# Kernel optimization log

Measured on AMD Instinct MI355X. Metric: run time of the kernel, lower is better.

The kernel has to match this reference:

```python
import jax, jax.numpy as jnp
import numpy as np
from jax import lax
from jax.scipy.special import logsumexp

B, N = 8, 2048
EPS = 0.2      # entropic regularization for Sinkhorn-EMD
ITERS = 20     # Sinkhorn iterations (CUDA EMD kernel is likewise an approximate matcher)


def setup_inputs() -> dict:
    key = jax.random.key(0)
    k1, k2 = jax.random.split(key)
    target = jax.random.normal(k1, (B, N, 3), dtype=jnp.float32)
    pre = jax.random.normal(k2, (B, N, 3), dtype=jnp.float32)
    return {"target": target, "pre": pre}


def _pairwise_sq(x, y):
    # x: [B,N,3], y: [B,M,3] -> squared L2 distances [B,N,M]
    xx = jnp.sum(x * x, axis=-1)                      # [B,N]
    yy = jnp.sum(y * y, axis=-1)                      # [B,M]
    xy = jnp.einsum('bnd,bmd->bnm', x, y)             # [B,N,M]
    return xx[:, :, None] + yy[:, None, :] - 2.0 * xy


def _total_loss(target, pre):
    C = _pairwise_sq(pre, target)                     # [B,N,M] cost: squared dists
    n, m = C.shape[1], C.shape[2]

    # Chamfer: chamfer_3DDist returns squared NN distances both ways.
    dist1 = jnp.min(C, axis=2)                        # pre -> target, [B,N]
    dist2 = jnp.min(C, axis=1)                        # target -> pre, [B,M]
    # per-sample cd = mean(dist1) + 0.5*mean(dist2), summed over batch
    cd_total = jnp.sum(jnp.mean(dist1, axis=1) + 0.5 * jnp.mean(dist2, axis=1))

    # EMD via entropic OT (Sinkhorn, log-domain) with uniform marginals.
    log_a = -jnp.log(jnp.float32(n))
    log_b = -jnp.log(jnp.float32(m))
    f0 = jnp.zeros((C.shape[0], n), dtype=C.dtype)
    g0 = jnp.zeros((C.shape[0], m), dtype=C.dtype)

    def step(carry, _):
        f, g = carry
        f = -EPS * logsumexp((g[:, None, :] - C) / EPS + log_b, axis=2)
        g = -EPS * logsumexp((f[:, :, None] - C) / EPS + log_a, axis=1)
        return (f, g), None

    (f, g), _ = lax.scan(step, (f0, g0), None, length=ITERS)
    logP = (f[:, :, None] + g[:, None, :] - C) / EPS + log_a + log_b
    # CUDA earth_mover_distance returns sum of matched squared dists per sample;
    # OT plan rows carry mass 1/n, so scale by n to get the per-point matching sum.
    emd_b = jnp.float32(n) * jnp.sum(jnp.exp(logP) * C, axis=(1, 2))  # [B]
    emd_loss = jnp.sum(emd_b)

    return cd_total + emd_loss


def reference(target, pre):
    return _total_loss(target, pre)
```

## Files before the change

### kernel.cpp

```cpp
#include <hip/hip_runtime.h>
#include <math.h>

#define NTHREADS 512
#define NPTS 2048
#define MSTEPS (NPTS / 64)
#define RPW 4
#define NWAVES (NTHREADS / 64)
#define ROWS_PER_BLOCK (NWAVES * RPW)
#define BLKB (NPTS / ROWS_PER_BLOCK)
#define BATCH 8
#define NBLOCKS (BATCH * BLKB)
#define SINK_ITERS 20

#if __has_builtin(__builtin_amdgcn_exp2f)
#define EXP2(x) __builtin_amdgcn_exp2f(x)
#else
#define EXP2(x) exp2f(x)
#endif

#define S2F 7.21347520444482f
#define LB2 -11.0f
#define FINAL_SCALE (0.13862943611198906f / 2048.0f)

#define WS_PART  0
#define WS_DONE  2048
#define WS_F     4096
#define WS_G     (WS_F    + 4 * BATCH * NPTS)
#define WS_CMIN  (WS_G    + 4 * BATCH * NPTS)
#define WS_PT    (WS_CMIN + 4 * BATCH * NPTS)
#define WS_PP    (WS_PT   + 16 * BATCH * NPTS)

static __device__ __forceinline__ float aload(const float* p) {
  return __hip_atomic_load(p, __ATOMIC_RELAXED, __HIP_MEMORY_SCOPE_AGENT);
}
static __device__ __forceinline__ unsigned aloadu(const unsigned* p) {
  return __hip_atomic_load(p, __ATOMIC_RELAXED, __HIP_MEMORY_SCOPE_AGENT);
}

__global__ void __launch_bounds__(256, 4)
prep_kernel(const float* __restrict__ target, const float* __restrict__ pre,
            unsigned char* __restrict__ ws)
{
  float4*   PT   = (float4*)(ws + WS_PT);
  float4*   PP   = (float4*)(ws + WS_PP);
  float*    F    = (float*)(ws + WS_F);
  float*    G    = (float*)(ws + WS_G);
  unsigned* CMIN = (unsigned*)(ws + WS_CMIN);
  unsigned* done = (unsigned*)(ws + WS_DONE);

  const float S1 = sqrtf(S2F);
  int gid = blockIdx.x * 256 + threadIdx.x;
  if (gid == 0) *done = 0u;
  if (gid < BATCH * NPTS) {
    const float* p = target + (size_t)gid * 3;
    float y0 = p[0] * S1, y1 = p[1] * S1, y2 = p[2] * S1;
    PT[gid] = make_float4(y0, y1, y2, y0 * y0 + y1 * y1 + y2 * y2);
    const float* q = pre + (size_t)gid * 3;
    float z0 = q[0] * S1, z1 = q[1] * S1, z2 = q[2] * S1;
    PP[gid] = make_float4(z0, z1, z2, z0 * z0 + z1 * z1 + z2 * z2);
    F[gid] = 0.0f;
    G[gid] = 0.0f;
    CMIN[gid] = 0x7f800000u;
  }
}

template<int MODE>
__global__ void __launch_bounds__(NTHREADS, 4)
sink_kernel(const float4* __restrict__ rowpts, const float4* __restrict__ colpts,
            const float* __restrict__ Vin, float* __restrict__ Vout,
            unsigned char* __restrict__ ws, float* __restrict__ out)
{
  float*    partial = (float*)(ws + WS_PART);
  unsigned* done    = (unsigned*)(ws + WS_DONE);
  unsigned* CMIN    = (unsigned*)(ws + WS_CMIN);

  __shared__ float4 cols4[NPTS];
  __shared__ float  W2[NPTS];
  __shared__ float  wsum[NWAVES];
  __shared__ int    isLast;

  const int tid  = threadIdx.x;
  const int wid  = tid >> 6;
  const int lane = tid & 63;
  const int b    = blockIdx.x / BLKB;
  const int bib  = blockIdx.x % BLKB;

  const float4* rb = rowpts + (size_t)b * NPTS;
  const float4* cb = colpts + (size_t)b * NPTS;
  const float*  Vi = (MODE == 1) ? nullptr : (Vin + (size_t)b * NPTS);
  float*        Vo = (MODE == 2) ? nullptr : (Vout + (size_t)b * NPTS);
  unsigned*     CMb = CMIN + (size_t)b * NPTS;

  for (int m = tid; m < NPTS; m += NTHREADS) {
    float4 p = cb[m];
    float w;
    if (MODE == 1) {
      w = LB2 - p.w;
      ((unsigned*)W2)[m] = 0x7f800000u;
    } else {
      float v = Vi[m];
      w = v - p.w + LB2;
      if (MODE == 2) W2[m] = v + LB2;
    }
    cols4[m] = make_float4(p.x, p.y, p.z, w);
  }
  __syncthreads();

  const int n0 = bib * ROWS_PER_BLOCK + wid * RPW;
  float x2[RPW][3], XX[RPW], S[RPW], tm[RPW], Sc[RPW];
#pragma unroll
  for (int r = 0; r < RPW; ++r) {
    float4 a = rb[n0 + r];
    XX[r] = a.w;
    x2[r][0] = a.x + a.x; x2[r][1] = a.y + a.y; x2[r][2] = a.z + a.z;
    S[r] = 0.0f;
    if (MODE == 1) tm[r] = -3.0e38f;
    if (MODE == 2) Sc[r] = 0.0f;
  }

#pragma unroll 2
  for (int ms = 0; ms < MSTEPS; ++ms) {
    float4 v = cols4[ms * 64 + lane];
    float w2;
    if (MODE == 2) w2 = W2[ms * 64 + lane];
    float tmax;
    if (MODE == 1) tmax = -3.0e38f;
#pragma unroll
    for (int r = 0; r < RPW; ++r) {
      float t = v.w - XX[r];
      t = fmaf(x2[r][0], v.x, t);
      t = fmaf(x2[r][1], v.y, t);
      t = fmaf(x2[r][2], v.z, t);
      float e = EXP2(t);
      S[r] += e;
      if (MODE == 1) { tm[r] = fmaxf(tm[r], t); tmax = fmaxf(tmax, t); }
      if (MODE == 2) { Sc[r] = fmaf(e, w2 - t, Sc[r]); }
    }
    if (MODE == 1)
      atomicMin((unsigned*)&W2[ms * 64 + lane], __float_as_uint(LB2 - tmax));
  }

  float rowacc = 0.0f;
#pragma unroll
  for (int r = 0; r < RPW; ++r) {
    float s = S[r];
    for (int off = 32; off; off >>= 1) s += __shfl_xor(s, off);
    if (MODE != 2) {
      if (lane == r) Vo[n0 + r] = -log2f(s);
    } else {
      float sc = Sc[r];
      for (int off = 32; off; off >>= 1) sc += __shfl_xor(sc, off);
      rowacc += 2048.0f * (sc / s);
    }
    if (MODE == 1) {
      float t = tm[r];
      for (int off = 32; off; off >>= 1) t = fmaxf(t, __shfl_xor(t, off));
      rowacc += LB2 - t;
    }
  }

  if (MODE == 1) {
    if (lane == 0) wsum[wid] = rowacc;
    __syncthreads();
    if (tid == 0) {
      float s = 0.0f;
#pragma unroll
      for (int w = 0; w < NWAVES; ++w) s += wsum[w];
      partial[blockIdx.x] = s;
    }
    for (int m = tid; m < NPTS; m += NTHREADS)
      atomicMin(&CMb[m], ((unsigned*)W2)[m]);
  }

  if (MODE == 2) {
    if (lane == 0) wsum[wid] = rowacc;
    __syncthreads();
    if (tid == 0) {
      float s = 0.0f;
#pragma unroll
      for (int w = 0; w < NWAVES; ++w) s += wsum[w];
      partial[blockIdx.x] += s;
      __threadfence();
      unsigned old = __hip_atomic_fetch_add(done, 1u, __ATOMIC_ACQ_REL,
                                            __HIP_MEMORY_SCOPE_AGENT);
      isLast = (old == (unsigned)NBLOCKS - 1u) ? 1 : 0;
    }
    __syncthreads();
    if (isLast) {
      float s = aload(&partial[tid]);
      for (int j = tid; j < BATCH * NPTS; j += NTHREADS)
        s += 0.5f * __uint_as_float(aloadu(&CMIN[j]));
      for (int off = 32; off; off >>= 1) s += __shfl_xor(s, off);
      if (lane == 0) wsum[wid] = s;
      __syncthreads();
      if (tid == 0) {
        float t = 0.0f;
#pragma unroll
        for (int w = 0; w < NWAVES; ++w) t += wsum[w];
        out[0] = t * FINAL_SCALE;
      }
    }
  }
}

extern "C" void kernel_launch(void* const* d_in, const int* in_sizes, int n_in,
                              void* d_out, int out_size, void* d_ws, size_t ws_size,
                              hipStream_t stream) {
  const float* target = (const float*)d_in[0];
  const float* pre    = (const float*)d_in[1];
  float* out = (float*)d_out;
  unsigned char* ws = (unsigned char*)d_ws;

  const float4* PT = (const float4*)(ws + WS_PT);
  const float4* PP = (const float4*)(ws + WS_PP);
  float* F = (float*)(ws + WS_F);
  float* G = (float*)(ws + WS_G);

  prep_kernel<<<dim3((BATCH * NPTS + 255) / 256), dim3(256), 0, stream>>>(target, pre, ws);

  sink_kernel<1><<<dim3(NBLOCKS), dim3(NTHREADS), 0, stream>>>(PP, PT, nullptr, F, ws, nullptr);
  sink_kernel<0><<<dim3(NBLOCKS), dim3(NTHREADS), 0, stream>>>(PT, PP, F, G, ws, nullptr);

  for (int it = 1; it < SINK_ITERS; ++it) {
    sink_kernel<0><<<dim3(NBLOCKS), dim3(NTHREADS), 0, stream>>>(PP, PT, G, F, ws, nullptr);
    if (it < SINK_ITERS - 1) {
      sink_kernel<0><<<dim3(NBLOCKS), dim3(NTHREADS), 0, stream>>>(PT, PP, F, G, ws, nullptr);
    } else {
      sink_kernel<2><<<dim3(NBLOCKS), dim3(NTHREADS), 0, stream>>>(PT, PP, F, nullptr, ws, out);
    }
  }
}
```

Baseline: 469.1 us.

## Fuse prep into first Sinkhorn pass and compute column Chamfer min in final pass

Removes the separate prep kernel: the first Sinkhorn kernel now reads the raw target/pre points, scales them, writes the packed float4 arrays for its own rows, and builds its column tile in shared memory. The target->pre Chamfer minimum is no longer gathered with per-column shared and global atomicMin plus a global CMIN buffer. It is computed as a per-row min in the final MODE 2 pass, which already iterates over the transposed orientation. This drops one launch, the CMIN init and readback, and the atomics, at the cost of extra fmin work in the last pass.

```diff
diff --git a/kernel.cpp b/kernel.cpp
--- a/kernel.cpp
+++ b/kernel.cpp
@@ -26,41 +26,94 @@
 #define WS_DONE  2048
 #define WS_F     4096
 #define WS_G     (WS_F    + 4 * BATCH * NPTS)
-#define WS_CMIN  (WS_G    + 4 * BATCH * NPTS)
-#define WS_PT    (WS_CMIN + 4 * BATCH * NPTS)
+#define WS_PT    (WS_G    + 4 * BATCH * NPTS)
 #define WS_PP    (WS_PT   + 16 * BATCH * NPTS)
 
 static __device__ __forceinline__ float aload(const float* p) {
   return __hip_atomic_load(p, __ATOMIC_RELAXED, __HIP_MEMORY_SCOPE_AGENT);
 }
-static __device__ __forceinline__ unsigned aloadu(const unsigned* p) {
-  return __hip_atomic_load(p, __ATOMIC_RELAXED, __HIP_MEMORY_SCOPE_AGENT);
-}
-
-__global__ void __launch_bounds__(256, 4)
-prep_kernel(const float* __restrict__ target, const float* __restrict__ pre,
-            unsigned char* __restrict__ ws)
+
+__global__ void __launch_bounds__(NTHREADS, 4)
+sink_first_kernel(const float* __restrict__ target, const float* __restrict__ pre,
+                  unsigned char* __restrict__ ws)
 {
-  float4*   PT   = (float4*)(ws + WS_PT);
-  float4*   PP   = (float4*)(ws + WS_PP);
-  float*    F    = (float*)(ws + WS_F);
-  float*    G    = (float*)(ws + WS_G);
-  unsigned* CMIN = (unsigned*)(ws + WS_CMIN);
-  unsigned* done = (unsigned*)(ws + WS_DONE);
-
+  float*    partial = (float*)(ws + WS_PART);
+  unsigned* done    = (unsigned*)(ws + WS_DONE);
+  float*    F       = (float*)(ws + WS_F);
+  float4*   PT      = (float4*)(ws + WS_PT);
+  float4*   PP      = (float4*)(ws + WS_PP);
+
+  __shared__ float4 cols4[NPTS];
+  __shared__ float  wsum[NWAVES];
+
+  const int tid  = threadIdx.x;
+  const int wid  = tid >> 6;
+  const int lane = tid & 63;
+  const int b    = blockIdx.x / BLKB;
+  const int bib  = blockIdx.x % BLKB;
   const float S1 = sqrtf(S2F);
-  int gid = blockIdx.x * 256 + threadIdx.x;
-  if (gid == 0) *done = 0u;
-  if (gid < BATCH * NPTS) {
-    const float* p = target + (size_t)gid * 3;
+
+  if (blockIdx.x == 0 && tid == 0) *done = 0u;
+
+  const float*  tb = target + (size_t)b * NPTS * 3;
+  const float*  pb = pre    + (size_t)b * NPTS * 3;
+  const unsigned mlo = (unsigned)(bib * ROWS_PER_BLOCK);
+
+  for (int m = tid; m < NPTS; m += NTHREADS) {
+    const float* p = tb + m * 3;
     float y0 = p[0] * S1, y1 = p[1] * S1, y2 = p[2] * S1;
-    PT[gid] = make_float4(y0, y1, y2, y0 * y0 + y1 * y1 + y2 * y2);
-    const float* q = pre + (size_t)gid * 3;
-    float z0 = q[0] * S1, z1 = q[1] * S1, z2 = q[2] * S1;
-    PP[gid] = make_float4(z0, z1, z2, z0 * z0 + z1 * z1 + z2 * z2);
-    F[gid] = 0.0f;
-    G[gid] = 0.0f;
-    CMIN[gid] = 0x7f800000u;
+    float yy = y0 * y0 + y1 * y1 + y2 * y2;
+    if ((unsigned)m - mlo < (unsigned)ROWS_PER_BLOCK)
+      PT[(size_t)b * NPTS + m] = make_float4(y0, y1, y2, yy);
+    cols4[m] = make_float4(y0, y1, y2, LB2 - yy);
+  }
+
+  const int n0 = (int)mlo + wid * RPW;
+  float x2[RPW][3], XX[RPW], S[RPW], tm[RPW];
+#pragma unroll
+  for (int r = 0; r < RPW; ++r) {
+    const float* q = pb + (size_t)(n0 + r) * 3;
+    float a0 = q[0] * S1, a1 = q[1] * S1, a2 = q[2] * S1;
+    float xx = a0 * a0 + a1 * a1 + a2 * a2;
+    if (lane == r) PP[(size_t)b * NPTS + n0 + r] = make_float4(a0, a1, a2, xx);
+    XX[r] = xx;
+    x2[r][0] = a0 + a0; x2[r][1] = a1 + a1; x2[r][2] = a2 + a2;
+    S[r] = 0.0f; tm[r] = -3.0e38f;
+  }
+  __syncthreads();
+
+#pragma unroll 2
+  for (int ms = 0; ms < MSTEPS; ++ms) {
+    float4 v = cols4[ms * 64 + lane];
+#pragma unroll
+    for (int r = 0; r < RPW; ++r) {
+      float t = v.w - XX[r];
+      t = fmaf(x2[r][0], v.x, t);
+      t = fmaf(x2[r][1], v.y, t);
+      t = fmaf(x2[r][2], v.z, t);
+      S[r] += EXP2(t);
+      tm[r] = fmaxf(tm[r], t);
+    }
+  }
+
+  float rowacc = 0.0f;
+  float* Fb = F + (size_t)b * NPTS;
+#pragma unroll
+  for (int r = 0; r < RPW; ++r) {
+    float s = S[r];
+    for (int off = 32; off; off >>= 1) s += __shfl_xor(s, off);
+    if (lane == r) Fb[n0 + r] = -log2f(s);
+    float t = tm[r];
+    for (int off = 32; off; off >>= 1) t = fmaxf(t, __shfl_xor(t, off));
+    rowacc += LB2 - t;
+  }
+  if (lane == 0) wsum[wid] = rowacc;
+  __syncthreads();
+  if (tid == 0) {
+    float s = 0.0f;
+#pragma unroll
+    for (int w = 0; w < NWAVES; ++w) s += wsum[w];
+    partial[blockIdx.x] = s;
   }
 }
 
@@ -72,10 +125,9 @@
 {
   float*    partial = (float*)(ws + WS_PART);
   unsigned* done    = (unsigned*)(ws + WS_DONE);
-  unsigned* CMIN    = (unsigned*)(ws + WS_CMIN);
 
   __shared__ float4 cols4[NPTS];
-  __shared__ float  W2[NPTS];
+  __shared__ float  W2[MODE == 2 ? NPTS : 1];
   __shared__ float  wsum[NWAVES];
   __shared__ int    isLast;
 
@@ -87,35 +139,26 @@
 
   const float4* rb = rowpts + (size_t)b * NPTS;
   const float4* cb = colpts + (size_t)b * NPTS;
-  const float*  Vi = (MODE == 1) ? nullptr : (Vin + (size_t)b * NPTS);
+  const float*  Vi = Vin + (size_t)b * NPTS;
   float*        Vo = (MODE == 2) ? nullptr : (Vout + (size_t)b * NPTS);
-  unsigned*     CMb = CMIN + (size_t)b * NPTS;
 
   for (int m = tid; m < NPTS; m += NTHREADS) {
     float4 p = cb[m];
-    float w;
-    if (MODE == 1) {
-      w = LB2 - p.w;
-      ((unsigned*)W2)[m] = 0x7f800000u;
-    } else {
-      float v = Vi[m];
-      w = v - p.w + LB2;
-      if (MODE == 2) W2[m] = v + LB2;
-    }
-    cols4[m] = make_float4(p.x, p.y, p.z, w);
+    float v = Vi[m];
+    if (MODE == 2) W2[m] = v + LB2;
+    cols4[m] = make_float4(p.x, p.y, p.z, v - p.w + LB2);
   }
   __syncthreads();
 
   const int n0 = bib * ROWS_PER_BLOCK + wid * RPW;
-  float x2[RPW][3], XX[RPW], S[RPW], tm[RPW], Sc[RPW];
+  float x2[RPW][3], XX[RPW], S[RPW], Sc[RPW], rm2[RPW];
 #pragma unroll
   for (int r = 0; r < RPW; ++r) {
     float4 a = rb[n0 + r];
     XX[r] = a.w;
     x2[r][0] = a.x + a.x; x2[r][1] = a.y + a.y; x2[r][2] = a.z + a.z;
     S[r] = 0.0f;
-    if (MODE == 1) tm[r] = -3.0e38f;
-    if (MODE == 2) Sc[r] = 0.0f;
+    if (MODE == 2) { Sc[r] = 0.0f; rm2[r] = 3.0e38f; }
   }
 
 #pragma unroll 2
@@ -123,8 +166,6 @@
     float4 v = cols4[ms * 64 + lane];
     float w2;
     if (MODE == 2) w2 = W2[ms * 64 + lane];
-    float tmax;
-    if (MODE == 1) tmax = -3.0e38f;
 #pragma unroll
     for (int r = 0; r < RPW; ++r) {
       float t = v.w - XX[r];
@@ -133,11 +174,12 @@
       t = fmaf(x2[r][2], v.z, t);
       float e = EXP2(t);
       S[r] += e;
-      if (MODE == 1) { tm[r] = fmaxf(tm[r], t); tmax = fmaxf(tmax, t); }
-      if (MODE == 2) { Sc[r] = fmaf(e, w2 - t, Sc[r]); }
-    }
-    if (MODE == 1)
-      atomicMin((unsigned*)&W2[ms * 64 + lane], __float_as_uint(LB2 - tmax));
+      if (MODE == 2) {
+        float c2 = w2 - t;
+        Sc[r] = fmaf(e, c2, Sc[r]);
+        rm2[r] = fminf(rm2[r], c2);
+      }
+    }
   }
 
   float rowacc = 0.0f;
@@ -150,26 +192,10 @@
     } else {
       float sc = Sc[r];
       for (int off = 32; off; off >>= 1) sc += __shfl_xor(sc, off);
-      rowacc += 2048.0f * (sc / s);
-    }
-    if (MODE == 1) {
-      float t = tm[r];
-      for (int off = 32; off; off >>= 1) t = fmaxf(t, __shfl_xor(t, off));
-      rowacc += LB2 - t;
-    }
-  }
-
-  if (MODE == 1) {
-    if (lane == 0) wsum[wid] = rowacc;
-    __syncthreads();
-    if (tid == 0) {
-      float s = 0.0f;
-#pragma unroll
-      for (int w = 0; w < NWAVES; ++w) s += wsum[w];
-      partial[blockIdx.x] = s;
-    }
-    for (int m = tid; m < NPTS; m += NTHREADS)
-      atomicMin(&CMb[m], ((unsigned*)W2)[m]);
+      float m2 = rm2[r];
+      for (int off = 32; off; off >>= 1) m2 = fminf(m2, __shfl_xor(m2, off));
+      rowacc += 2048.0f * (sc / s) + 0.5f * m2;
+    }
   }
 
   if (MODE == 2) {
@@ -188,8 +214,6 @@
     __syncthreads();
     if (isLast) {
       float s = aload(&partial[tid]);
-      for (int j = tid; j < BATCH * NPTS; j += NTHREADS)
-        s += 0.5f * __uint_as_float(aloadu(&CMIN[j]));
       for (int off = 32; off; off >>= 1) s += __shfl_xor(s, off);
       if (lane == 0) wsum[wid] = s;
       __syncthreads();
@@ -216,9 +240,7 @@
   float* F = (float*)(ws + WS_F);
   float* G = (float*)(ws + WS_G);
 
-  prep_kernel<<<dim3((BATCH * NPTS + 255) / 256), dim3(256), 0, stream>>>(target, pre, ws);
-
-  sink_kernel<1><<<dim3(NBLOCKS), dim3(NTHREADS), 0, stream>>>(PP, PT, nullptr, F, ws, nullptr);
+  sink_first_kernel<<<dim3(NBLOCKS), dim3(NTHREADS), 0, stream>>>(target, pre, ws);
   sink_kernel<0><<<dim3(NBLOCKS), dim3(NTHREADS), 0, stream>>>(PT, PP, F, G, ws, nullptr);
 
   for (int it = 1; it < SINK_ITERS; ++it) {
```

Result: no change. 460.9 us (-1.7%).
